# Performance work log

Hardware: AMD Instinct MI355X
Metric: run time of the kernel (lower is better)

Reference implementation:

```python
import jax, jax.numpy as jnp
import numpy as np

B, T, L, H, NH, F, V, K = 8, 128, 12, 768, 12, 3072, 30522, 5
DH = H // NH
START, STOP = 3, 4  # tag_to_idx['<START>'], tag_to_idx['<STOP>']


def _ln(x, s, b):
    m = jnp.mean(x, -1, keepdims=True)
    v = jnp.var(x, -1, keepdims=True)
    return (x - m) * jax.lax.rsqrt(v + 1e-12) * s + b


def setup_inputs() -> dict:
    key = jax.random.key(0)
    ks = jax.random.split(key, 16)
    sc = 0.02
    rn = lambda k, shp: jax.random.normal(k, shp, jnp.float32) * sc
    inp = {
        'sentence': jax.random.randint(ks[0], (B, T), 0, V),
        'sentence_mask': jnp.ones((B, T), jnp.int32),
        'word_emb': rn(ks[1], (V, H)),
        'pos_emb': rn(ks[2], (T, H)),
        'type_emb': rn(ks[3], (2, H)),
        'emb_ln_s': jnp.ones((H,), jnp.float32),
        'emb_ln_b': jnp.zeros((H,), jnp.float32),
        'Wqkv': rn(ks[4], (L, H, 3 * H)), 'bqkv': jnp.zeros((L, 3 * H), jnp.float32),
        'Wo': rn(ks[5], (L, H, H)), 'bo': jnp.zeros((L, H), jnp.float32),
        'ln1_s': jnp.ones((L, H), jnp.float32), 'ln1_b': jnp.zeros((L, H), jnp.float32),
        'W1': rn(ks[6], (L, H, F)), 'b1': jnp.zeros((L, F), jnp.float32),
        'W2': rn(ks[7], (L, F, H)), 'b2': jnp.zeros((L, H), jnp.float32),
        'ln2_s': jnp.ones((L, H), jnp.float32), 'ln2_b': jnp.zeros((L, H), jnp.float32),
        'Wt': rn(ks[8], (H, K)), 'bt': jnp.zeros((K,), jnp.float32),
    }
    trans = jax.random.normal(ks[9], (K, K), jnp.float32)
    # transitions[START, :] = -10000 ; transitions[:, STOP] = -10000
    trans = trans.at[START, :].set(-10000.0).at[:, STOP].set(-10000.0)
    inp['transitions'] = trans
    return inp


def _bert_feats(sentence, sentence_mask, word_emb, pos_emb, type_emb,
                emb_ln_s, emb_ln_b, Wqkv, bqkv, Wo, bo, ln1_s, ln1_b,
                W1, b1, W2, b2, ln2_s, ln2_b, Wt, bt):
    # embeddings (token_type_ids=None -> all zeros)
    x = word_emb[sentence] + pos_emb[None, :, :] + type_emb[0][None, None, :]
    x = _ln(x, emb_ln_s, emb_ln_b)
    # additive attention bias from padding mask
    bias = (1.0 - sentence_mask.astype(jnp.float32))[:, None, None, :] * -10000.0
    inv_sqrt_dh = 1.0 / np.sqrt(DH)

    def layer(h, p):
        wqkv, bqk, wo, bo_, s1, sb1, w1, wb1, w2, wb2, s2, sb2 = p
        qkv = h @ wqkv + bqk
        q, k, v = jnp.split(qkv, 3, axis=-1)
        q = q.reshape(B, T, NH, DH)
        k = k.reshape(B, T, NH, DH)
        v = v.reshape(B, T, NH, DH)
        att = jnp.einsum('bqhd,bkhd->bhqk', q, k) * inv_sqrt_dh + bias
        att = jax.nn.softmax(att, axis=-1)
        ctx = jnp.einsum('bhqk,bkhd->bqhd', att, v).reshape(B, T, H)
        h = _ln(h + ctx @ wo + bo_, s1, sb1)
        ff = jax.nn.gelu(h @ w1 + wb1) @ w2 + wb2
        h = _ln(h + ff, s2, sb2)
        return h, None

    x, _ = jax.lax.scan(layer, x, (Wqkv, bqkv, Wo, bo, ln1_s, ln1_b,
                                   W1, b1, W2, b2, ln2_s, ln2_b))
    # dropout(p=0.2) is identity at inference
    return x @ Wt + bt  # [B, T, K]


def _viterbi(feats, transitions):
    # feats: [B, T, K]; transitions[to, from]
    init = jnp.full((B, K), -10000.0, feats.dtype).at[:, START].set(0.0)

    def fwd_step(ld, feat_t):
        m = transitions[None, :, :] + ld[:, None, :]  # [B, K(to), K(from)]
        best = jnp.max(m, axis=-1)
        psi_t = jnp.argmax(m, axis=-1)
        return best + feat_t, psi_t

    feats_t = jnp.swapaxes(feats, 0, 1)  # [T, B, K]
    ld, psis = jax.lax.scan(fwd_step, init, feats_t[1:])  # psis: [T-1, B, K]
    score = jnp.max(ld, axis=-1)          # [B]
    last = jnp.argmax(ld, axis=-1)        # [B]

    def bwd_step(p, psi_t):
        prev = jnp.take_along_axis(psi_t, p[:, None], axis=-1)[:, 0]
        return prev, prev

    _, rest = jax.lax.scan(bwd_step, last, psis, reverse=True)  # [T-1, B]
    path = jnp.concatenate([rest, last[None, :]], axis=0).T     # [B, T]
    return score, path


def reference(sentence, sentence_mask, word_emb, pos_emb, type_emb,
              emb_ln_s, emb_ln_b, Wqkv, bqkv, Wo, bo, ln1_s, ln1_b,
              W1, b1, W2, b2, ln2_s, ln2_b, Wt, bt, transitions):
    feats = _bert_feats(sentence, sentence_mask, word_emb, pos_emb, type_emb,
                        emb_ln_s, emb_ln_b, Wqkv, bqkv, Wo, bo, ln1_s, ln1_b,
                        W1, b1, W2, b2, ln2_s, ln2_b, Wt, bt)
    score, path = _viterbi(feats, transitions)
    return score, path
```

## Files before the change

kernel.cpp:

```cpp
#include <hip/hip_runtime.h>
#include <cstdint>
#include <cstddef>

#define BB 8
#define TT 128
#define LL 12
#define HH 768
#define NHH 12
#define DHH 64
#define FFI 3072
#define KT 5
#define START_TAG 3
#define MTOK (BB*TT)

typedef _Float16 f16x8 __attribute__((ext_vector_type(8)));
typedef _Float16 f16x4 __attribute__((ext_vector_type(4)));
typedef float f32x4 __attribute__((ext_vector_type(4)));

__device__ __forceinline__ void gl_lds16(const _Float16* g, _Float16* l) {
    __builtin_amdgcn_global_load_lds(
        (const __attribute__((address_space(1))) unsigned int*)g,
        (__attribute__((address_space(3))) unsigned int*)l, 16, 0, 0);
}

__device__ __forceinline__ float gelu_f(float x) {
    float c = 0.7978845608028654f * (x + 0.044715f * x * x * x);
    return 0.5f * x * (1.f + tanhf(c));
}

__device__ __forceinline__ void write_h_planes(const float* rowbuf, int tok,
                                               _Float16* dh, _Float16* dl, int c) {
    int kb = c >> 2;
    int rowm = tok & 127, mb = tok >> 7;
    int koct = c & 3;
    int p = rowm * 4 + (koct ^ (rowm & 3));
    size_t tb = ((size_t)(mb * 24 + kb)) * 4096;
    f16x8 vh, vl;
#pragma unroll
    for (int j = 0; j < 8; ++j) {
        float x = rowbuf[c * 8 + j];
        _Float16 hi = (_Float16)x;
        vh[j] = hi;
        vl[j] = (_Float16)((x - (float)hi) * 4096.f);
    }
    *(f16x8*)(dh + tb + (size_t)p * 8) = vh;
    *(f16x8*)(dl + tb + (size_t)p * 8) = vl;
}

__global__ __launch_bounds__(256) void embed_ln_kernel(
    const int* __restrict__ sentence,
    const float* __restrict__ word_emb,
    const float* __restrict__ pos_emb,
    const float* __restrict__ type_emb,
    const float* __restrict__ ln_s,
    const float* __restrict__ ln_b,
    float* __restrict__ h,
    _Float16* __restrict__ dh, _Float16* __restrict__ dl)
{
    int tok = blockIdx.x;
    int t = tok % TT;
    int id = sentence[tok];
    const float* we = word_emb + (size_t)id * HH;
    const float* pe = pos_emb + (size_t)t * HH;

    __shared__ float rowbuf[HH];
    __shared__ float rs_[4], rss_[4];
    float x[3];
    float s = 0.f, ss = 0.f;
#pragma unroll
    for (int i = 0; i < 3; ++i) {
        int d = threadIdx.x + i * 256;
        float v = we[d] + pe[d] + type_emb[d];
        x[i] = v; s += v; ss += v * v;
    }
    for (int o = 32; o; o >>= 1) { s += __shfl_down(s, o); ss += __shfl_down(ss, o); }
    int wid = threadIdx.x >> 6;
    if ((threadIdx.x & 63) == 0) { rs_[wid] = s; rss_[wid] = ss; }
    __syncthreads();
    s = rs_[0] + rs_[1] + rs_[2] + rs_[3];
    ss = rss_[0] + rss_[1] + rss_[2] + rss_[3];
    float mean = s * (1.f / HH);
    float var = ss * (1.f / HH) - mean * mean;
    float rstd = rsqrtf(var + 1e-12f);
#pragma unroll
    for (int i = 0; i < 3; ++i) {
        int d = threadIdx.x + i * 256;
        float y = (x[i] - mean) * rstd * ln_s[d] + ln_b[d];
        h[(size_t)tok * HH + d] = y;
        rowbuf[d] = y;
    }
    __syncthreads();
    if (threadIdx.x < 96) write_h_planes(rowbuf, tok, dh, dl, threadIdx.x);
}

template<int FEATS>
__global__ __launch_bounds__(256) void add_ln_red_kernel(
    float* __restrict__ h, const float* __restrict__ parts,
    const float* __restrict__ bias,
    const float* __restrict__ ln_s, const float* __restrict__ ln_b,
    _Float16* __restrict__ dh, _Float16* __restrict__ dl,
    const float* __restrict__ Wt, const float* __restrict__ bt,
    float* __restrict__ feats)
{
    int tok = blockIdx.x;
    __shared__ float rowbuf[HH];
    __shared__ float rs_[4], rss_[4];
    float x[3];
    float s = 0.f, ss = 0.f;
#pragma unroll
    for (int i = 0; i < 3; ++i) {
        int d = threadIdx.x + i * 256;
        size_t idx = (size_t)tok * HH + d;
        float delta = parts[idx] + parts[idx + (size_t)MTOK * HH]
                    + parts[idx + 2 * (size_t)MTOK * HH] + parts[idx + 3 * (size_t)MTOK * HH]
                    + bias[d];
        float v = h[idx] + delta;
        x[i] = v; s += v; ss += v * v;
    }
    for (int o = 32; o; o >>= 1) { s += __shfl_down(s, o); ss += __shfl_down(ss, o); }
    int wid = threadIdx.x >> 6;
    if ((threadIdx.x & 63) == 0) { rs_[wid] = s; rss_[wid] = ss; }
    __syncthreads();
    s = rs_[0] + rs_[1] + rs_[2] + rs_[3];
    ss = rss_[0] + rss_[1] + rss_[2] + rss_[3];
    float mean = s * (1.f / HH);
    float var = ss * (1.f / HH) - mean * mean;
    float rstd = rsqrtf(var + 1e-12f);
    float yv[3];
#pragma unroll
    for (int i = 0; i < 3; ++i) {
        int d = threadIdx.x + i * 256;
        float y = (x[i] - mean) * rstd * ln_s[d] + ln_b[d];
        yv[i] = y;
        if constexpr (!FEATS) {
            h[(size_t)tok * HH + d] = y;
            rowbuf[d] = y;
        }
    }
    if constexpr (!FEATS) {
        __syncthreads();
        if (threadIdx.x < 96) write_h_planes(rowbuf, tok, dh, dl, threadIdx.x);
    } else {
        float pt[5] = {0.f, 0.f, 0.f, 0.f, 0.f};
#pragma unroll
        for (int i = 0; i < 3; ++i) {
            int d = threadIdx.x + i * 256;
#pragma unroll
            for (int t = 0; t < 5; ++t) pt[t] += yv[i] * Wt[d * 5 + t];
        }
#pragma unroll
        for (int t = 0; t < 5; ++t)
            for (int o = 32; o; o >>= 1) pt[t] += __shfl_down(pt[t], o);
        __shared__ float fred[4][5];
        if ((threadIdx.x & 63) == 0)
#pragma unroll
            for (int t = 0; t < 5; ++t) fred[wid][t] = pt[t];
        __syncthreads();
        if (threadIdx.x < 5) {
            float fs = fred[0][threadIdx.x] + fred[1][threadIdx.x]
                     + fred[2][threadIdx.x] + fred[3][threadIdx.x] + bt[threadIdx.x];
            feats[tok * 5 + threadIdx.x] = fs;
        }
    }
}

__global__ __launch_bounds__(256) void wconv_kernel(
    const float* __restrict__ Wqkv, const float* __restrict__ Wo,
    const float* __restrict__ W1, const float* __restrict__ W2,
    _Float16* __restrict__ qh, _Float16* __restrict__ ql,
    _Float16* __restrict__ oh, _Float16* __restrict__ ol,
    _Float16* __restrict__ f1h, _Float16* __restrict__ f1l,
    _Float16* __restrict__ f2h, _Float16* __restrict__ f2l)
{
    int b = blockIdx.x;
    const float* src; _Float16 *dh, *dl; int N, kTi, idx;
    if (b < 864)       { idx = b;        src = Wqkv; dh = qh;  dl = ql;  N = 2304; kTi = 24; }
    else if (b < 1152) { idx = b - 864;  src = Wo;   dh = oh;  dl = ol;  N = 768;  kTi = 24; }
    else if (b < 2304) { idx = b - 1152; src = W1;   dh = f1h; dl = f1l; N = 3072; kTi = 24; }
    else               { idx = b - 2304; src = W2;   dh = f2h; dl = f2l; N = 768;  kTi = 96; }
    int nb = idx / kTi, kb = idx % kTi;

    __shared__ float tile[32][65];
    const float* s0 = src + (size_t)(kb * 32) * N + nb * 64;
#pragma unroll
    for (int i = 0; i < 8; ++i) {
        int q = threadIdx.x + i * 256;
        int kk = q >> 6, n = q & 63;
        tile[kk][n] = s0[(size_t)kk * N + n];
    }
    __syncthreads();
    int p = threadIdx.x;
    int n = p >> 2, koct = (p & 3) ^ (n & 3);
    f16x8 vh, vl;
#pragma unroll
    for (int j = 0; j < 8; ++j) {
        float x = tile[koct * 8 + j][n];
        _Float16 hi = (_Float16)x;
        vh[j] = hi;
        vl[j] = (_Float16)((x - (float)hi) * 4096.f);
    }
    size_t tb = (size_t)idx * 2048;
    *(f16x8*)(dh + tb + (size_t)p * 8) = vh;
    *(f16x8*)(dl + tb + (size_t)p * 8) = vl;
}

template<int MODE>
__global__ __launch_bounds__(256) void mfma_gemm(
    const _Float16* __restrict__ Ah, const _Float16* __restrict__ Al,
    const _Float16* __restrict__ Bh, const _Float16* __restrict__ Bl,
    const float* __restrict__ bias, float* __restrict__ outF,
    _Float16* __restrict__ o1h, _Float16* __restrict__ o1l,
    _Float16* __restrict__ o2h, _Float16* __restrict__ o2l,
    int N, int kTi, int kpz)
{
    constexpr bool TRANS = (MODE >= 2);
    __shared__ _Float16 lds[2][12288];
    int tid = threadIdx.x, lane = tid & 63, w = tid >> 6;
    int wm = w >> 1, wn = w & 1;
    int mb = blockIdx.y, nb = blockIdx.x;
    int ktBeg = TRANS ? 0 : blockIdx.z * kpz;
    int ktEnd = TRANS ? kTi : ktBeg + kpz;

    const _Float16 *aTh, *aTl, *bTh, *bTl;
    if constexpr (!TRANS) {
        aTh = Ah + (size_t)mb * kTi * 4096;
        aTl = Al + (size_t)mb * kTi * 4096;
        bTh = Bh + (size_t)nb * kTi * 2048;
        bTl = Bl + (size_t)nb * kTi * 2048;
    } else {
        aTh = Ah + (size_t)(2 * mb) * kTi * 2048;
        aTl = Al + (size_t)(2 * mb) * kTi * 2048;
        bTh = Bh + (size_t)(nb >> 1) * kTi * 4096 + (nb & 1) * 2048;
        bTl = Bl + (size_t)(nb >> 1) * kTi * 4096 + (nb & 1) * 2048;
    }

    f32x4 acch[4][2], accc[4][2];
#pragma unroll
    for (int i = 0; i < 4; ++i)
#pragma unroll
        for (int j = 0; j < 2; ++j) { acch[i][j] = (f32x4)0.f; accc[i][j] = (f32x4)0.f; }

    auto stage = [&](int buf, int kt) {
#pragma unroll
        for (int j = 0; j < 6; ++j) {
            int i = w * 6 + j;
            const _Float16* src;
            if constexpr (!TRANS) {
                if (i < 8)       src = aTh + (size_t)kt * 4096 + i * 512;
                else if (i < 16) src = aTl + (size_t)kt * 4096 + (i - 8) * 512;
                else if (i < 20) src = bTh + (size_t)kt * 2048 + (i - 16) * 512;
                else             src = bTl + (size_t)kt * 2048 + (i - 20) * 512;
            } else {
                if (i < 8)       src = aTh + (size_t)(i >> 2) * kTi * 2048 + (size_t)kt * 2048 + (i & 3) * 512;
                else if (i < 16) src = aTl + (size_t)((i - 8) >> 2) * kTi * 2048 + (size_t)kt * 2048 + ((i - 8) & 3) * 512;
                else if (i < 20) src = bTh + (size_t)kt * 4096 + (i - 16) * 512;
                else             src = bTl + (size_t)kt * 4096 + (i - 20) * 512;
            }
            gl_lds16(src + lane * 8, &lds[buf][i * 512]);
        }
    };

    stage(0, ktBeg);
    stage(1, ktBeg + 1);
    int lm = lane & 15, lk = lane >> 4;
    for (int kt = ktBeg; kt < ktEnd; ++kt) {
        int cur = (kt - ktBeg) & 1;
        if (kt + 1 < ktEnd) { asm volatile("s_waitcnt vmcnt(6)" ::: "memory"); }
        else                { asm volatile("s_waitcnt vmcnt(0)" ::: "memory"); }
        __builtin_amdgcn_sched_barrier(0);
        __builtin_amdgcn_s_barrier();
        __builtin_amdgcn_sched_barrier(0);
        const char* lb = (const char*)&lds[cur][0];
        f16x8 ahf[4], alf[4], bhf[2], blf[2];
#pragma unroll
        for (int mi = 0; mi < 4; ++mi) {
            int row = wm * 64 + mi * 16 + lm;
            int off = (row * 64 + lk * 16) ^ ((row & 3) << 4);
            ahf[mi] = *(const f16x8*)(lb + off);
            alf[mi] = *(const f16x8*)(lb + 8192 + off);
        }
#pragma unroll
        for (int ni = 0; ni < 2; ++ni) {
            int nr = wn * 32 + ni * 16 + lm;
            int off = (nr * 64 + lk * 16) ^ ((nr & 3) << 4);
            bhf[ni] = *(const f16x8*)(lb + 16384 + off);
            blf[ni] = *(const f16x8*)(lb + 20480 + off);
        }
        asm volatile("s_waitcnt lgkmcnt(0)" ::: "memory");
        __builtin_amdgcn_sched_barrier(0);
        __builtin_amdgcn_s_barrier();
        __builtin_amdgcn_sched_barrier(0);
        if (kt + 2 < ktEnd) stage(cur, kt + 2);
#pragma unroll
        for (int mi = 0; mi < 4; ++mi)
#pragma unroll
            for (int ni = 0; ni < 2; ++ni) {
                acch[mi][ni] = __builtin_amdgcn_mfma_f32_16x16x32_f16(ahf[mi], bhf[ni], acch[mi][ni], 0, 0, 0);
                accc[mi][ni] = __builtin_amdgcn_mfma_f32_16x16x32_f16(ahf[mi], blf[ni], accc[mi][ni], 0, 0, 0);
                accc[mi][ni] = __builtin_amdgcn_mfma_f32_16x16x32_f16(alf[mi], bhf[ni], accc[mi][ni], 0, 0, 0);
            }
    }

    const float inv = 1.0f / 4096.0f;
    if constexpr (MODE == 0) {
        float* Cz = outF + (size_t)blockIdx.z * 1024 * N;
#pragma unroll
        for (int mi = 0; mi < 4; ++mi)
#pragma unroll
            for (int ni = 0; ni < 2; ++ni) {
                int col = nb * 64 + wn * 32 + ni * 16 + lm;
                int r0 = mb * 128 + wm * 64 + mi * 16 + lk * 4;
#pragma unroll
                for (int j = 0; j < 4; ++j)
                    Cz[(size_t)(r0 + j) * N + col] = acch[mi][ni][j] + accc[mi][ni][j] * inv;
            }
    } else if constexpr (MODE == 2) {
        int region = mb / 6;
#pragma unroll
        for (int mi = 0; mi < 4; ++mi)
#pragma unroll
            for (int ni = 0; ni < 2; ++ni) {
                int n = mb * 128 + wm * 64 + mi * 16 + lk * 4;
                int tok = nb * 64 + wn * 32 + ni * 16 + lm;
                float4 bv = *(const float4*)(bias + n);
                float v[4];
#pragma unroll
                for (int j = 0; j < 4; ++j)
                    v[j] = acch[mi][ni][j] + accc[mi][ni][j] * inv + (&bv.x)[j];
                int b = tok >> 7, q = tok & 127;
                if (region < 2) {
                    int hh2 = (n >> 6) % 12, d = n & 63;
                    size_t img = (size_t)(b * 12 + hh2);
                    _Float16* dsth = (region == 0) ? o1h : o2h;
                    _Float16* dstl = (region == 0) ? o1l : o2l;
                    int byteo = q * 128 + ((d * 2) ^ ((q & 7) << 4));
                    f16x4 hi, lo;
#pragma unroll
                    for (int j = 0; j < 4; ++j) {
                        _Float16 hv = (_Float16)v[j];
                        hi[j] = hv; lo[j] = (_Float16)((v[j] - (float)hv) * 4096.f);
                    }
                    *(f16x4*)((char*)dsth + img * 16384 + byteo) = hi;
                    *(f16x4*)((char*)dstl + img * 16384 + byteo) = lo;
                } else {
                    int hh2 = (n - 1536) >> 6, d = n & 63;
                    float* vdst = outF + (size_t)(b * 12 + hh2) * 8192;
#pragma unroll
                    for (int j = 0; j < 4; ++j)
                        vdst[(size_t)(d + j) * 128 + q] = v[j];
                }
            }
    } else {
#pragma unroll
        for (int mi = 0; mi < 4; ++mi)
#pragma unroll
            for (int ni = 0; ni < 2; ++ni) {
                int n = mb * 128 + wm * 64 + mi * 16 + lk * 4;
                int tok = nb * 64 + wn * 32 + ni * 16 + lm;
                float4 bv = *(const float4*)(bias + n);
                int mbt = tok >> 7, rowm = tok & 127;
                int kb = n >> 5, koct = (n >> 3) & 3, half = (n >> 2) & 1;
                size_t eo = ((size_t)(mbt * 96 + kb)) * 4096
                          + (size_t)(rowm * 4 + (koct ^ (rowm & 3))) * 8 + half * 4;
                f16x4 hi, lo;
#pragma unroll
                for (int j = 0; j < 4; ++j) {
                    float x = gelu_f(acch[mi][ni][j] + accc[mi][ni][j] * inv + (&bv.x)[j]);
                    _Float16 hv = (_Float16)x;
                    hi[j] = hv; lo[j] = (_Float16)((x - (float)hv) * 4096.f);
                }
                *(f16x4*)(o1h + eo) = hi;
                *(f16x4*)(o1l + eo) = lo;
            }
    }
}

__global__ __launch_bounds__(256, 1) void attn_mfma(
    const _Float16* __restrict__ Qp_h, const _Float16* __restrict__ Qp_l,
    const _Float16* __restrict__ Kp_h, const _Float16* __restrict__ Kp_l,
    const float* __restrict__ vT, const int* __restrict__ mask,
    _Float16* __restrict__ cA_h, _Float16* __restrict__ cA_l)
{
    __shared__ __align__(16) char sm[82432];
    char* Kh  = sm;             char* Klo = sm + 16384;
    char* Qh  = sm + 32768;     char* Qlo = sm + 40960;
    char* Ph  = sm;             char* Plo = sm + 16384;
    char* Vth = sm + 49152;     char* Vtl = sm + 65536;
    float* biasf = (float*)(sm + 81920);

    int bx = blockIdx.x;
    int bh = bx >> 1, qh2 = bx & 1;
    int b = bh / 12, h = bh % 12;
    int q0 = qh2 * 64;
    int tid = threadIdx.x, lane = tid & 63, wv = tid >> 6;
    int lm = lane & 15, g = lane >> 4;
    int qr = wv * 16 + lm;
    const float inv = 1.0f / 4096.0f;

    {
        const _Float16* Ksh = Kp_h + (size_t)bh * 8192;
        const _Float16* Ksl = Kp_l + (size_t)bh * 8192;
        const _Float16* Qsh = Qp_h + (size_t)bh * 8192 + (size_t)q0 * 64;
        const _Float16* Qsl = Qp_l + (size_t)bh * 8192 + (size_t)q0 * 64;
#pragma unroll
        for (int i = 0; i < 4; ++i) {
            gl_lds16(Ksh + (size_t)(i * 256 + tid) * 8, (_Float16*)(Kh  + (i * 256 + tid) * 16));
            gl_lds16(Ksl + (size_t)(i * 256 + tid) * 8, (_Float16*)(Klo + (i * 256 + tid) * 16));
        }
#pragma unroll
        for (int i = 0; i < 2; ++i) {
            gl_lds16(Qsh + (size_t)(i * 256 + tid) * 8, (_Float16*)(Qh  + (i * 256 + tid) * 16));
            gl_lds16(Qsl + (size_t)(i * 256 + tid) * 8, (_Float16*)(Qlo + (i * 256 + tid) * 16));
        }
    }
    if (tid < 128) biasf[tid] = (1.f - (float)mask[b * 128 + tid]) * -10000.f;
    __syncthreads();

    f32x4 ah[8], ac[8];
#pragma unroll
    for (int i = 0; i < 8; ++i) { ah[i] = (f32x4)0.f; ac[i] = (f32x4)0.f; }
    __builtin_amdgcn_s_setprio(1);
#pragma unroll
    for (int ks = 0; ks < 2; ++ks) {
        int qoff = qr * 128 + ((ks * 64 + g * 16) ^ ((qr & 7) << 4));
        f16x8 q_h = *(const f16x8*)(Qh + qoff);
        f16x8 q_l = *(const f16x8*)(Qlo + qoff);
#pragma unroll
        for (int mf = 0; mf < 8; ++mf) {
            int kt = mf * 16 + lm;
            int koff = kt * 128 + ((ks * 64 + g * 16) ^ ((kt & 7) << 4));
            f16x8 k_h = *(const f16x8*)(Kh + koff);
            f16x8 k_l = *(const f16x8*)(Klo + koff);
            ah[mf] = __builtin_amdgcn_mfma_f32_16x16x32_f16(k_h, q_h, ah[mf], 0, 0, 0);
            ac[mf] = __builtin_amdgcn_mfma_f32_16x16x32_f16(k_h, q_l, ac[mf], 0, 0, 0);
            ac[mf] = __builtin_amdgcn_mfma_f32_16x16x32_f16(k_l, q_h, ac[mf], 0, 0, 0);
        }
    }
    __builtin_amdgcn_s_setprio(0);

    float kb_[8][4];
#pragma unroll
    for (int mf = 0; mf < 8; ++mf)
#pragma unroll
        for (int jj = 0; jj < 4; ++jj) kb_[mf][jj] = biasf[mf * 16 + g * 4 + jj];

    float pv_[8][4];
    float mx = -1e30f;
#pragma unroll
    for (int mf = 0; mf < 8; ++mf)
#pragma unroll
        for (int jj = 0; jj < 4; ++jj) {
            float s = (ah[mf][jj] + ac[mf][jj] * inv) * 0.125f + kb_[mf][jj];
            pv_[mf][jj] = s;
            mx = fmaxf(mx, s);
        }
    mx = fmaxf(mx, __shfl_xor(mx, 16));
    mx = fmaxf(mx, __shfl_xor(mx, 32));
    float sum = 0.f;
#pragma unroll
    for (int mf = 0; mf < 8; ++mf)
#pragma unroll
        for (int jj = 0; jj < 4; ++jj) {
            float e = expf(pv_[mf][jj] - mx);
            pv_[mf][jj] = e;
            sum += e;
        }
    sum += __shfl_xor(sum, 16);
    sum += __shfl_xor(sum, 32);
    float rs = 1.f / sum;
    __syncthreads();

#pragma unroll
    for (int mf = 0; mf < 8; ++mf) {
        f16x4 hi, lo;
#pragma unroll
        for (int jj = 0; jj < 4; ++jj) {
            float p = pv_[mf][jj] * rs;
            _Float16 hv = (_Float16)p;
            hi[jj] = hv; lo[jj] = (_Float16)((p - (float)hv) * 4096.f);
        }
        int byteo = qr * 256 + ((mf * 32 + g * 8) ^ ((qr & 7) << 4));
        *(f16x4*)(Ph + byteo) = hi;
        *(f16x4*)(Plo + byteo) = lo;
    }
    {
        int d = tid >> 2, tb = (tid & 3) * 32;
        const float* vsrc = vT + (size_t)bh * 8192 + (size_t)d * 128 + tb;
#pragma unroll
        for (int i = 0; i < 8; ++i) {
            float4 v = *(const float4*)(vsrc + i * 4);
            f16x4 hi, lo;
#pragma unroll
            for (int jj = 0; jj < 4; ++jj) {
                float x = (&v.x)[jj];
                _Float16 hv = (_Float16)x;
                hi[jj] = hv; lo[jj] = (_Float16)((x - (float)hv) * 4096.f);
            }
            int byteo = d * 256 + (((tb + i * 4) * 2) ^ ((d & 7) << 4));
            *(f16x4*)(Vth + byteo) = hi;
            *(f16x4*)(Vtl + byteo) = lo;
        }
    }
    __syncthreads();

    f32x4 ch[4], cc[4];
#pragma unroll
    for (int i = 0; i < 4; ++i) { ch[i] = (f32x4)0.f; cc[i] = (f32x4)0.f; }
    __builtin_amdgcn_s_setprio(1);
#pragma unroll
    for (int ks = 0; ks < 4; ++ks) {
        int poff = qr * 256 + ((ks * 64 + g * 16) ^ ((qr & 7) << 4));
        f16x8 p_h = *(const f16x8*)(Ph + poff);
        f16x8 p_l = *(const f16x8*)(Plo + poff);
#pragma unroll
        for (int mf = 0; mf < 4; ++mf) {
            int d = mf * 16 + lm;
            int voff = d * 256 + ((ks * 64 + g * 16) ^ ((d & 7) << 4));
            f16x8 vh = *(const f16x8*)(Vth + voff);
            f16x8 vl = *(const f16x8*)(Vtl + voff);
            ch[mf] = __builtin_amdgcn_mfma_f32_16x16x32_f16(vh, p_h, ch[mf], 0, 0, 0);
            cc[mf] = __builtin_amdgcn_mfma_f32_16x16x32_f16(vh, p_l, cc[mf], 0, 0, 0);
            cc[mf] = __builtin_amdgcn_mfma_f32_16x16x32_f16(vl, p_h, cc[mf], 0, 0, 0);
        }
    }
    __builtin_amdgcn_s_setprio(0);

    int q = q0 + qr;
#pragma unroll
    for (int mf = 0; mf < 4; ++mf) {
        int d0 = mf * 16 + g * 4;
        f16x4 hi, lo;
#pragma unroll
        for (int jj = 0; jj < 4; ++jj) {
            float x = ch[mf][jj] + cc[mf][jj] * inv;
            _Float16 hv = (_Float16)x;
            hi[jj] = hv; lo[jj] = (_Float16)((x - (float)hv) * 4096.f);
        }
        int kb = h * 2 + (d0 >> 5), koct = (d0 >> 3) & 3, half = (d0 >> 2) & 1;
        size_t eo = ((size_t)(b * 24 + kb)) * 4096
                  + (size_t)(q * 4 + (koct ^ (q & 3))) * 8 + half * 4;
        *(f16x4*)(cA_h + eo) = hi;
        *(f16x4*)(cA_l + eo) = lo;
    }
}

__global__ __launch_bounds__(64) void viterbi_kernel(
    const float* __restrict__ feats, const float* __restrict__ trans,
    float* __restrict__ out)
{
    __shared__ float tr[KT][KT];
    __shared__ unsigned char psi[TT - 1][BB][KT];
    int tid = threadIdx.x;
    if (tid < KT * KT) tr[tid / KT][tid % KT] = trans[tid];
    __syncthreads();
    if (tid < BB) {
        int b = tid;
        float ld[KT];
#pragma unroll
        for (int k = 0; k < KT; ++k) ld[k] = (k == START_TAG) ? 0.f : -10000.f;
        for (int t = 1; t < TT; ++t) {
            float nld[KT];
#pragma unroll
            for (int to = 0; to < KT; ++to) {
                float best = tr[to][0] + ld[0];
                int arg = 0;
#pragma unroll
                for (int fr = 1; fr < KT; ++fr) {
                    float v = tr[to][fr] + ld[fr];
                    if (v > best) { best = v; arg = fr; }
                }
                psi[t - 1][b][to] = (unsigned char)arg;
                nld[to] = best + feats[(size_t)(b * TT + t) * KT + to];
            }
#pragma unroll
            for (int k = 0; k < KT; ++k) ld[k] = nld[k];
        }
        float sc = ld[0]; int last = 0;
#pragma unroll
        for (int k = 1; k < KT; ++k) if (ld[k] > sc) { sc = ld[k]; last = k; }
        out[b] = sc;
        int p = last;
        out[BB + b * TT + (TT - 1)] = (float)last;
        for (int t = TT - 2; t >= 0; --t) {
            p = psi[t][b][p];
            out[BB + b * TT + t] = (float)p;
        }
    }
}

extern "C" void kernel_launch(void* const* d_in, const int* in_sizes, int n_in,
                              void* d_out, int out_size, void* d_ws, size_t ws_size,
                              hipStream_t stream) {
    const int*   sentence = (const int*)d_in[0];
    const int*   mask     = (const int*)d_in[1];
    const float* word_emb = (const float*)d_in[2];
    const float* pos_emb  = (const float*)d_in[3];
    const float* type_emb = (const float*)d_in[4];
    const float* emb_ln_s = (const float*)d_in[5];
    const float* emb_ln_b = (const float*)d_in[6];
    const float* Wqkv     = (const float*)d_in[7];
    const float* bqkv     = (const float*)d_in[8];
    const float* Wo       = (const float*)d_in[9];
    const float* bo       = (const float*)d_in[10];
    const float* ln1_s    = (const float*)d_in[11];
    const float* ln1_b    = (const float*)d_in[12];
    const float* W1       = (const float*)d_in[13];
    const float* b1       = (const float*)d_in[14];
    const float* W2       = (const float*)d_in[15];
    const float* b2       = (const float*)d_in[16];
    const float* ln2_s    = (const float*)d_in[17];
    const float* ln2_b    = (const float*)d_in[18];
    const float* Wt       = (const float*)d_in[19];
    const float* bt       = (const float*)d_in[20];
    const float* trans    = (const float*)d_in[21];

    char* base = (char*)d_ws;
    size_t off = 0;
    auto alloc = [&](size_t bytes) { void* p = base + off; off += (bytes + 255) & ~(size_t)255; return p; };

    _Float16* wq_h = (_Float16*)alloc(768u * 2304 * 2);
    _Float16* wq_l = (_Float16*)alloc(768u * 2304 * 2);
    _Float16* wo_h = (_Float16*)alloc(768u * 768 * 2);
    _Float16* wo_l = (_Float16*)alloc(768u * 768 * 2);
    _Float16* w1_h = (_Float16*)alloc(768u * 3072 * 2);
    _Float16* w1_l = (_Float16*)alloc(768u * 3072 * 2);
    _Float16* w2_h = (_Float16*)alloc(3072u * 768 * 2);
    _Float16* w2_l = (_Float16*)alloc(3072u * 768 * 2);
    float* h       = (float*)alloc((size_t)MTOK * HH * 4);
    _Float16* hA_h = (_Float16*)alloc((size_t)MTOK * HH * 2);
    _Float16* hA_l = (_Float16*)alloc((size_t)MTOK * HH * 2);
    _Float16* Qp_h = (_Float16*)alloc((size_t)96 * 8192 * 2);
    _Float16* Qp_l = (_Float16*)alloc((size_t)96 * 8192 * 2);
    _Float16* Kp_h = (_Float16*)alloc((size_t)96 * 8192 * 2);
    _Float16* Kp_l = (_Float16*)alloc((size_t)96 * 8192 * 2);
    float* vT      = (float*)alloc((size_t)96 * 8192 * 4);
    _Float16* cA_h = (_Float16*)alloc((size_t)MTOK * HH * 2);
    _Float16* cA_l = (_Float16*)alloc((size_t)MTOK * HH * 2);
    _Float16* gA_h = (_Float16*)alloc((size_t)MTOK * FFI * 2);
    _Float16* gA_l = (_Float16*)alloc((size_t)MTOK * FFI * 2);
    float* parts   = (float*)alloc((size_t)4 * MTOK * HH * 4);
    float* featsb  = (float*)alloc((size_t)MTOK * KT * 4);

    embed_ln_kernel<<<MTOK, 256, 0, stream>>>(sentence, word_emb, pos_emb, type_emb,
                                              emb_ln_s, emb_ln_b, h, hA_h, hA_l);
    for (int l = 0; l < LL; ++l) {
        wconv_kernel<<<3456, 256, 0, stream>>>(
            Wqkv + (size_t)l * 768 * 2304, Wo + (size_t)l * 768 * 768,
            W1 + (size_t)l * 768 * 3072, W2 + (size_t)l * 3072 * 768,
            wq_h, wq_l, wo_h, wo_l, w1_h, w1_l, w2_h, w2_l);
        mfma_gemm<2><<<dim3(16, 18), 256, 0, stream>>>(
            wq_h, wq_l, hA_h, hA_l, bqkv + (size_t)l * 2304, vT,
            Qp_h, Qp_l, Kp_h, Kp_l, 0, 24, 24);
        attn_mfma<<<192, 256, 0, stream>>>(Qp_h, Qp_l, Kp_h, Kp_l, vT, mask, cA_h, cA_l);
        mfma_gemm<0><<<dim3(12, 8, 4), 256, 0, stream>>>(
            cA_h, cA_l, wo_h, wo_l, nullptr, parts,
            nullptr, nullptr, nullptr, nullptr, 768, 24, 6);
        add_ln_red_kernel<0><<<MTOK, 256, 0, stream>>>(
            h, parts, bo + (size_t)l * HH, ln1_s + (size_t)l * HH, ln1_b + (size_t)l * HH,
            hA_h, hA_l, nullptr, nullptr, nullptr);
        mfma_gemm<3><<<dim3(16, 24), 256, 0, stream>>>(
            w1_h, w1_l, hA_h, hA_l, b1 + (size_t)l * FFI, nullptr,
            gA_h, gA_l, nullptr, nullptr, 0, 24, 24);
        mfma_gemm<0><<<dim3(12, 8, 4), 256, 0, stream>>>(
            gA_h, gA_l, w2_h, w2_l, nullptr, parts,
            nullptr, nullptr, nullptr, nullptr, 768, 96, 24);
        if (l < LL - 1) {
            add_ln_red_kernel<0><<<MTOK, 256, 0, stream>>>(
                h, parts, b2 + (size_t)l * HH, ln2_s + (size_t)l * HH, ln2_b + (size_t)l * HH,
                hA_h, hA_l, nullptr, nullptr, nullptr);
        } else {
            add_ln_red_kernel<1><<<MTOK, 256, 0, stream>>>(
                h, parts, b2 + (size_t)l * HH, ln2_s + (size_t)l * HH, ln2_b + (size_t)l * HH,
                hA_h, hA_l, Wt, bt, featsb);
        }
    }
    viterbi_kernel<<<1, 64, 0, stream>>>(featsb, trans, (float*)d_out);
}
```

Baseline: 1.516 ms.

## Convert all layer weights in one launch and drop a GEMM k-loop barrier

When the workspace is large enough, a single wconv launch splits the weights of all 12 layers into fp16 hi/lo planes up front. This replaces twelve per-layer conversion launches, and the GEMMs then index the per-layer planes by offset. Separately, the GEMM main loop drops the lgkmcnt wait and the barrier between the LDS fragment reads and the MFMAs. The next prefetch stage is now issued after the MFMAs behind a single barrier, so each k-step has one fewer barrier but prefetch starts later. The all-layer path needs a much larger workspace and falls back to per-layer conversion otherwise.

```diff
diff --git a/kernel.cpp b/kernel.cpp
--- a/kernel.cpp
+++ b/kernel.cpp
@@ -12,6 +12,11 @@
 #define KT 5
 #define START_TAG 3
 #define MTOK (BB*TT)
+
+#define LQS 1769472u
+#define LOS 589824u
+#define L1S 2359296u
+#define L2S 2359296u
 
 typedef _Float16 f16x8 __attribute__((ext_vector_type(8)));
 typedef _Float16 f16x4 __attribute__((ext_vector_type(4)));
@@ -164,6 +169,7 @@
     }
 }
 
+template<int ALL>
 __global__ __launch_bounds__(256) void wconv_kernel(
     const float* __restrict__ Wqkv, const float* __restrict__ Wo,
     const float* __restrict__ W1, const float* __restrict__ W2,
@@ -172,12 +178,14 @@
     _Float16* __restrict__ f1h, _Float16* __restrict__ f1l,
     _Float16* __restrict__ f2h, _Float16* __restrict__ f2l)
 {
-    int b = blockIdx.x;
+    int bb = blockIdx.x;
+    int l = ALL ? bb / 3456 : 0;
+    int b = ALL ? bb % 3456 : bb;
     const float* src; _Float16 *dh, *dl; int N, kTi, idx;
-    if (b < 864)       { idx = b;        src = Wqkv; dh = qh;  dl = ql;  N = 2304; kTi = 24; }
-    else if (b < 1152) { idx = b - 864;  src = Wo;   dh = oh;  dl = ol;  N = 768;  kTi = 24; }
-    else if (b < 2304) { idx = b - 1152; src = W1;   dh = f1h; dl = f1l; N = 3072; kTi = 24; }
-    else               { idx = b - 2304; src = W2;   dh = f2h; dl = f2l; N = 768;  kTi = 96; }
+    if (b < 864)       { idx = b;        src = Wqkv + (size_t)l * 768 * 2304; dh = qh  + (size_t)l * LQS; dl = ql  + (size_t)l * LQS; N = 2304; kTi = 24; }
+    else if (b < 1152) { idx = b - 864;  src = Wo   + (size_t)l * 768 * 768;  dh = oh  + (size_t)l * LOS; dl = ol  + (size_t)l * LOS; N = 768;  kTi = 24; }
+    else if (b < 2304) { idx = b - 1152; src = W1   + (size_t)l * 768 * 3072; dh = f1h + (size_t)l * L1S; dl = f1l + (size_t)l * L1S; N = 3072; kTi = 24; }
+    else               { idx = b - 2304; src = W2   + (size_t)l * 3072 * 768; dh = f2h + (size_t)l * L2S; dl = f2l + (size_t)l * L2S; N = 768;  kTi = 96; }
     int nb = idx / kTi, kb = idx % kTi;
 
     __shared__ float tile[32][65];
@@ -267,7 +275,6 @@
         int cur = (kt - ktBeg) & 1;
         if (kt + 1 < ktEnd) { asm volatile("s_waitcnt vmcnt(6)" ::: "memory"); }
         else                { asm volatile("s_waitcnt vmcnt(0)" ::: "memory"); }
-        __builtin_amdgcn_sched_barrier(0);
         __builtin_amdgcn_s_barrier();
         __builtin_amdgcn_sched_barrier(0);
         const char* lb = (const char*)&lds[cur][0];
@@ -286,11 +293,6 @@
             bhf[ni] = *(const f16x8*)(lb + 16384 + off);
             blf[ni] = *(const f16x8*)(lb + 20480 + off);
         }
-        asm volatile("s_waitcnt lgkmcnt(0)" ::: "memory");
-        __builtin_amdgcn_sched_barrier(0);
-        __builtin_amdgcn_s_barrier();
-        __builtin_amdgcn_sched_barrier(0);
-        if (kt + 2 < ktEnd) stage(cur, kt + 2);
 #pragma unroll
         for (int mi = 0; mi < 4; ++mi)
 #pragma unroll
@@ -299,6 +301,9 @@
                 accc[mi][ni] = __builtin_amdgcn_mfma_f32_16x16x32_f16(ahf[mi], blf[ni], accc[mi][ni], 0, 0, 0);
                 accc[mi][ni] = __builtin_amdgcn_mfma_f32_16x16x32_f16(alf[mi], bhf[ni], accc[mi][ni], 0, 0, 0);
             }
+        __builtin_amdgcn_sched_barrier(0);
+        __builtin_amdgcn_s_barrier();
+        if (kt + 2 < ktEnd) stage(cur, kt + 2);
     }
 
     const float inv = 1.0f / 4096.0f;
@@ -618,14 +623,18 @@
     size_t off = 0;
     auto alloc = [&](size_t bytes) { void* p = base + off; off += (bytes + 255) & ~(size_t)255; return p; };
 
-    _Float16* wq_h = (_Float16*)alloc(768u * 2304 * 2);
-    _Float16* wq_l = (_Float16*)alloc(768u * 2304 * 2);
-    _Float16* wo_h = (_Float16*)alloc(768u * 768 * 2);
-    _Float16* wo_l = (_Float16*)alloc(768u * 768 * 2);
-    _Float16* w1_h = (_Float16*)alloc(768u * 3072 * 2);
-    _Float16* w1_l = (_Float16*)alloc(768u * 3072 * 2);
-    _Float16* w2_h = (_Float16*)alloc(3072u * 768 * 2);
-    _Float16* w2_l = (_Float16*)alloc(3072u * 768 * 2);
+    const size_t planeElems = (size_t)(LQS + LOS + L1S + L2S);
+    bool allL = ws_size >= (planeElems * 12 * 2 * 2 + (size_t)120 * 1024 * 1024);
+    int NLL = allL ? 12 : 1;
+
+    _Float16* wq_h = (_Float16*)alloc((size_t)LQS * NLL * 2);
+    _Float16* wq_l = (_Float16*)alloc((size_t)LQS * NLL * 2);
+    _Float16* wo_h = (_Float16*)alloc((size_t)LOS * NLL * 2);
+    _Float16* wo_l = (_Float16*)alloc((size_t)LOS * NLL * 2);
+    _Float16* w1_h = (_Float16*)alloc((size_t)L1S * NLL * 2);
+    _Float16* w1_l = (_Float16*)alloc((size_t)L1S * NLL * 2);
+    _Float16* w2_h = (_Float16*)alloc((size_t)L2S * NLL * 2);
+    _Float16* w2_l = (_Float16*)alloc((size_t)L2S * NLL * 2);
     float* h       = (float*)alloc((size_t)MTOK * HH * 4);
     _Float16* hA_h = (_Float16*)alloc((size_t)MTOK * HH * 2);
     _Float16* hA_l = (_Float16*)alloc((size_t)MTOK * HH * 2);
@@ -643,26 +652,37 @@
 
     embed_ln_kernel<<<MTOK, 256, 0, stream>>>(sentence, word_emb, pos_emb, type_emb,
                                               emb_ln_s, emb_ln_b, h, hA_h, hA_l);
+    if (allL) {
+        wconv_kernel<1><<<41472, 256, 0, stream>>>(
+            Wqkv, Wo, W1, W2,
+            wq_h, wq_l, wo_h, wo_l, w1_h, w1_l, w2_h, w2_l);
+    }
     for (int l = 0; l < LL; ++l) {
-        wconv_kernel<<<3456, 256, 0, stream>>>(
-            Wqkv + (size_t)l * 768 * 2304, Wo + (size_t)l * 768 * 768,
-            W1 + (size_t)l * 768 * 3072, W2 + (size_t)l * 3072 * 768,
-            wq_h, wq_l, wo_h, wo_l, w1_h, w1_l, w2_h, w2_l);
+        size_t qO = allL ? (size_t)l * LQS : 0;
+        size_t oO = allL ? (size_t)l * LOS : 0;
+        size_t f1O = allL ? (size_t)l * L1S : 0;
+        size_t f2O = allL ? (size_t)l * L2S : 0;
+        if (!allL) {
+            wconv_kernel<0><<<3456, 256, 0, stream>>>(
+                Wqkv + (size_t)l * 768 * 2304, Wo + (size_t)l * 768 * 768,
+                W1 + (size_t)l * 768 * 3072, W2 + (size_t)l * 3072 * 768,
+                wq_h, wq_l, wo_h, wo_l, w1_h, w1_l, w2_h, w2_l);
+        }
         mfma_gemm<2><<<dim3(16, 18), 256, 0, stream>>>(
-            wq_h, wq_l, hA_h, hA_l, bqkv + (size_t)l * 2304, vT,
+            wq_h + qO, wq_l + qO, hA_h, hA_l, bqkv + (size_t)l * 2304, vT,
             Qp_h, Qp_l, Kp_h, Kp_l, 0, 24, 24);
         attn_mfma<<<192, 256, 0, stream>>>(Qp_h, Qp_l, Kp_h, Kp_l, vT, mask, cA_h, cA_l);
         mfma_gemm<0><<<dim3(12, 8, 4), 256, 0, stream>>>(
-            cA_h, cA_l, wo_h, wo_l, nullptr, parts,
+            cA_h, cA_l, wo_h + oO, wo_l + oO, nullptr, parts,
             nullptr, nullptr, nullptr, nullptr, 768, 24, 6);
         add_ln_red_kernel<0><<<MTOK, 256, 0, stream>>>(
             h, parts, bo + (size_t)l * HH, ln1_s + (size_t)l * HH, ln1_b + (size_t)l * HH,
             hA_h, hA_l, nullptr, nullptr, nullptr);
         mfma_gemm<3><<<dim3(16, 24), 256, 0, stream>>>(
-            w1_h, w1_l, hA_h, hA_l, b1 + (size_t)l * FFI, nullptr,
+            w1_h + f1O, w1_l + f1O, hA_h, hA_l, b1 + (size_t)l * FFI, nullptr,
             gA_h, gA_l, nullptr, nullptr, 0, 24, 24);
         mfma_gemm<0><<<dim3(12, 8, 4), 256, 0, stream>>>(
-            gA_h, gA_l, w2_h, w2_l, nullptr, parts,
+            gA_h, gA_l, w2_h + f2O, w2_l + f2O, nullptr, parts,
             nullptr, nullptr, nullptr, nullptr, 768, 96, 24);
         if (l < LL - 1) {
             add_ln_red_kernel<0><<<MTOK, 256, 0, stream>>>(
```

Measured after the change: 1.543 ms. Within noise of the previous version (+1.8%).
